# Optimization experiments

Measured on AMD Instinct MI355X. Metric: run time of the kernel, lower is better.

## Reference

```python
import jax, jax.numpy as jnp
import numpy as np
import math

S, B, H, NH, HD = 2048, 1, 4096, 32, 128
ROT = HD // 2  # 2D RoPE: each half of head_dim gets its own rotary embedding


def _rotate_half(x):
    x1, x2 = jnp.split(x, 2, axis=-1)
    return jnp.concatenate((-x2, x1), axis=-1)


def _rope_tables(max_pos, dim):
    inv_freq = 1.0 / (10000.0 ** (jnp.arange(0, dim, 2, dtype=jnp.float32) / dim))
    freqs = jnp.arange(max_pos, dtype=jnp.float32)[:, None] * inv_freq[None, :]  # [P, dim/2]
    emb = jnp.concatenate((freqs, freqs), axis=-1)  # [P, dim]
    return jnp.cos(emb), jnp.sin(emb)


def _apply_rope(q, k, cos_t, sin_t, pid):
    # q,k: [S,B,NH,ROT]; pid: [S,B]
    c = cos_t[pid][:, :, None, :]  # [S,B,1,ROT]
    s = sin_t[pid][:, :, None, :]
    return q * c + _rotate_half(q) * s, k * c + _rotate_half(k) * s


def setup_inputs() -> dict:
    key = jax.random.key(0)
    k1, k2, k3, k4, k5 = jax.random.split(key, 5)
    hidden_states = jax.random.normal(k1, (S, B, H), dtype=jnp.float32)
    pos = jnp.arange(S, dtype=jnp.int32)[None, :]          # [1,S] standard positions
    blk = jnp.zeros((1, S), dtype=jnp.int32)                # block positions (pre-gmask all zeros)
    position_ids = jnp.stack([pos, blk], axis=1)            # [B,2,S]
    # causal mask: True = masked out
    attention_mask = jnp.triu(jnp.ones((S, S), dtype=bool), k=1)[None, None]  # [B,1,S,S]
    Wqkv = jax.random.normal(k2, (3 * H, H), dtype=jnp.float32) * 0.02
    bqkv = jax.random.normal(k3, (3 * H,), dtype=jnp.float32) * 0.02
    Wd = jax.random.normal(k4, (H, H), dtype=jnp.float32) * 0.02
    bd = jax.random.normal(k5, (H,), dtype=jnp.float32) * 0.02
    return {"hidden_states": hidden_states, "position_ids": position_ids,
            "attention_mask": attention_mask, "layer_id": 5,
            "Wqkv": Wqkv, "bqkv": bqkv, "Wd": Wd, "bd": bd}


def reference(hidden_states, position_ids, attention_mask, layer_id, Wqkv, bqkv, Wd, bd):
    # QKV projection: [S,B,H] -> [S,B,NH,3*HD]
    mixed = hidden_states @ Wqkv.T + bqkv
    mixed = mixed.reshape(S, B, NH, 3 * HD)
    q, k, v = jnp.split(mixed, 3, axis=-1)  # each [S,B,NH,HD]

    # 2D rotary position embedding on the two head-dim halves
    q1, q2 = jnp.split(q, 2, axis=-1)
    k1, k2 = jnp.split(k, 2, axis=-1)
    cos_t, sin_t = _rope_tables(S, ROT)
    pid = position_ids[:, 0, :].T   # [S,B]
    bid = position_ids[:, 1, :].T   # [S,B]
    q1, k1 = _apply_rope(q1, k1, cos_t, sin_t, pid)
    q2, k2 = _apply_rope(q2, k2, cos_t, sin_t, bid)
    q = jnp.concatenate([q1, q2], axis=-1)
    k = jnp.concatenate([k1, k2], axis=-1)

    # layer-scaled attention scores
    coeff = float(layer_id + 1)
    q = q / (math.sqrt(HD) * coeff)
    scores = jnp.einsum('sbnd,tbnd->bnst', q, k)  # [B,NH,S,S]
    scores = jnp.where(attention_mask, jnp.float32(-10000.0), scores)
    scores = scores.astype(jnp.float32) * coeff
    probs = jax.nn.softmax(scores, axis=-1).astype(hidden_states.dtype)

    ctx = jnp.einsum('bnst,tbnd->sbnd', probs, v).reshape(S, B, NH * HD)
    return ctx @ Wd.T + bd  # [S,B,H]
```

## Files before the change

kernel.cpp:

```cpp
#include <hip/hip_runtime.h>


#define S_LEN 2048
#define NHEAD 32
#define HDIM 128
#define HID 4096

typedef float f32x4 __attribute__((ext_vector_type(4)));
typedef __bf16 bf16x8 __attribute__((ext_vector_type(8)));
typedef __bf16 bf16x4 __attribute__((ext_vector_type(4)));
typedef _Float16 f16x4 __attribute__((ext_vector_type(4)));
typedef _Float16 f16x8 __attribute__((ext_vector_type(8)));

__device__ __forceinline__ void gload16(const void* g, void* l) {
  __builtin_amdgcn_global_load_lds(
      (const __attribute__((address_space(1))) void*)g,
      (__attribute__((address_space(3))) void*)l, 16, 0, 0);
}

__global__ __launch_bounds__(256) void cvt_f32_bf16_kernel(
    const float* __restrict__ in, __bf16* __restrict__ out, int n4) {
  int i = blockIdx.x * 256 + threadIdx.x;
  if (i >= n4) return;
  f32x4 v = *(const f32x4*)(in + (size_t)i * 4);
  bf16x4 o;
  o[0] = (__bf16)v[0]; o[1] = (__bf16)v[1];
  o[2] = (__bf16)v[2]; o[3] = (__bf16)v[3];
  *(bf16x4*)(out + (size_t)i * 4) = o;
}

template <int UNITS>
__device__ __forceinline__ void stage_rows(const __bf16* __restrict__ G,
                                           int grow0, int Kstride, int kofs,
                                           __bf16* lds, int tid) {
#pragma unroll
  for (int i = 0; i < UNITS; ++i) {
    int idx = i * 512 + tid;
    int rr = idx >> 3;
    int offp = (idx & 7) * 16;
    int off = offp ^ ((rr & 7) << 4);
    const char* src =
        (const char*)(G + (size_t)(grow0 + rr) * Kstride + kofs) + off;
    char* dst = (char*)lds + idx * 16;
    gload16(src, dst);
  }
}

__device__ __forceinline__ bf16x8 ldsfrag(const __bf16* hb, int rowin, int ks,
                                          int lg) {
  int off = ((ks * 64 + lg * 16) ^ ((rowin & 7) << 4));
  return *(const bf16x8*)((const char*)hb + rowin * 128 + off);
}

#define BAR asm volatile("s_barrier" ::: "memory");

__global__ __launch_bounds__(512, 2) void gemm192_kernel(
    const __bf16* __restrict__ A, const __bf16* __restrict__ B,
    const float* __restrict__ bias, __bf16* __restrict__ Cout, int M, int N,
    int K, int mtiles) {
  __shared__ __align__(16) __bf16 As[2][256 * 64];
  __shared__ __align__(16) __bf16 Bs[2][192 * 64];
  const int tid = threadIdx.x;
  int bid = blockIdx.x;
  int per_patch = mtiles * 8;
  int p = bid / per_patch, r = bid % per_patch;
  int mt = r % mtiles, nt = p * 8 + r / mtiles;
  int m0 = mt * 256, n0 = nt * 192;
  const int wid = tid >> 6, l = tid & 63;
  const int wm = wid >> 1, wn = wid & 1;
  const int lr = l & 15, lg = l >> 4;
  const int nk = K >> 6;

  f32x4 acc[4][6];
#pragma unroll
  for (int a = 0; a < 4; ++a)
#pragma unroll
    for (int b = 0; b < 6; ++b) acc[a][b] = 0.f;

  stage_rows<4>(A, m0, K, 0, &As[0][0], tid);
  stage_rows<3>(B, n0, K, 0, &Bs[0][0], tid);
  stage_rows<4>(A, m0, K, 64, &As[1][0], tid);
  stage_rows<3>(B, n0, K, 64, &Bs[1][0], tid);
  asm volatile("s_waitcnt vmcnt(7)" ::: "memory");
  BAR;

  for (int t = 0; t < nk; ++t) {
    const int cur = t & 1;
    const int kt2 = (t + 2) * 64;
    const bool s2 = (t + 2 < nk);
    bf16x8 a0[4], b0[6], a1[4], b1[6];

#pragma unroll
    for (int mi = 0; mi < 4; ++mi)
      a0[mi] = ldsfrag(&As[cur][0], wm * 64 + mi * 16 + lr, 0, lg);
#pragma unroll
    for (int nj = 0; nj < 6; ++nj)
      b0[nj] = ldsfrag(&Bs[cur][0], wn * 96 + nj * 16 + lr, 0, lg);
    BAR;
    __builtin_amdgcn_s_setprio(1);
#pragma unroll
    for (int mi = 0; mi < 4; ++mi)
#pragma unroll
      for (int nj = 0; nj < 6; ++nj)
        acc[mi][nj] = __builtin_amdgcn_mfma_f32_16x16x32_bf16(
            a0[mi], b0[nj], acc[mi][nj], 0, 0, 0);
    __builtin_amdgcn_s_setprio(0);

#pragma unroll
    for (int mi = 0; mi < 4; ++mi)
      a1[mi] = ldsfrag(&As[cur][0], wm * 64 + mi * 16 + lr, 1, lg);
#pragma unroll
    for (int nj = 0; nj < 6; ++nj)
      b1[nj] = ldsfrag(&Bs[cur][0], wn * 96 + nj * 16 + lr, 1, lg);
    BAR;
    if (s2) {
      stage_rows<4>(A, m0, K, kt2, &As[cur][0], tid);
      stage_rows<3>(B, n0, K, kt2, &Bs[cur][0], tid);
    }
    __builtin_amdgcn_s_setprio(1);
#pragma unroll
    for (int mi = 0; mi < 4; ++mi)
#pragma unroll
      for (int nj = 0; nj < 6; ++nj)
        acc[mi][nj] = __builtin_amdgcn_mfma_f32_16x16x32_bf16(
            a1[mi], b1[nj], acc[mi][nj], 0, 0, 0);
    __builtin_amdgcn_s_setprio(0);
    if (s2)
      asm volatile("s_waitcnt vmcnt(7)" ::: "memory");
    else
      asm volatile("s_waitcnt vmcnt(0)" ::: "memory");
  }

#pragma unroll
  for (int mi = 0; mi < 4; ++mi)
#pragma unroll
    for (int nj = 0; nj < 6; ++nj) {
      int row = m0 + wm * 64 + mi * 16 + lg * 4;
      int col = n0 + wn * 96 + nj * 16 + lr;
      float bv = bias[col];
      f32x4 v = acc[mi][nj];
#pragma unroll
      for (int j = 0; j < 4; ++j)
        Cout[(size_t)(row + j) * N + col] = (__bf16)(v[j] + bv);
    }
}

__global__ __launch_bounds__(512, 2) void gemm128_kernel(
    const __bf16* __restrict__ A, const __bf16* __restrict__ B,
    const float* __restrict__ bias, float* __restrict__ Cout, int M, int N,
    int K, int mtiles) {
  __shared__ __align__(16) __bf16 As[2][128 * 64];
  __shared__ __align__(16) __bf16 Bs[2][2][128 * 64];
  const int tid = threadIdx.x;
  int bid = blockIdx.x;
  int per_patch = mtiles * 8;
  int p = bid / per_patch, r = bid % per_patch;
  int mt = r % mtiles, nt = p * 8 + r / mtiles;
  int m0 = mt * 128, n0 = nt * 256;
  const int wid = tid >> 6, l = tid & 63;
  const int wm = wid >> 2, wn = wid & 3;
  const int lr = l & 15, lg = l >> 4;
  const int nk = K >> 6;

  f32x4 acc[4][4];
#pragma unroll
  for (int a = 0; a < 4; ++a)
#pragma unroll
    for (int b = 0; b < 4; ++b) acc[a][b] = 0.f;

  const int bhalf = wn >> 1;
  const int br0 = (wn & 1) * 64;

  stage_rows<2>(A, m0, K, 0, &As[0][0], tid);
  stage_rows<2>(B, n0, K, 0, &Bs[0][0][0], tid);
  stage_rows<2>(B, n0 + 128, K, 0, &Bs[0][1][0], tid);
  stage_rows<2>(A, m0, K, 64, &As[1][0], tid);
  stage_rows<2>(B, n0, K, 64, &Bs[1][0][0], tid);
  stage_rows<2>(B, n0 + 128, K, 64, &Bs[1][1][0], tid);
  asm volatile("s_waitcnt vmcnt(6)" ::: "memory");
  BAR;

  for (int t = 0; t < nk; ++t) {
    const int cur = t & 1;
    const int kt2 = (t + 2) * 64;
    const bool s2 = (t + 2 < nk);
    const __bf16* bslot = &Bs[cur][bhalf][0];
    bf16x8 a0[4], b0[4], a1[4], b1[4];

#pragma unroll
    for (int mi = 0; mi < 4; ++mi)
      a0[mi] = ldsfrag(&As[cur][0], wm * 64 + mi * 16 + lr, 0, lg);
#pragma unroll
    for (int nj = 0; nj < 4; ++nj)
      b0[nj] = ldsfrag(bslot, br0 + nj * 16 + lr, 0, lg);
    BAR;
    __builtin_amdgcn_s_setprio(1);
#pragma unroll
    for (int mi = 0; mi < 4; ++mi)
#pragma unroll
      for (int nj = 0; nj < 4; ++nj)
        acc[mi][nj] = __builtin_amdgcn_mfma_f32_16x16x32_bf16(
            a0[mi], b0[nj], acc[mi][nj], 0, 0, 0);
    __builtin_amdgcn_s_setprio(0);

#pragma unroll
    for (int mi = 0; mi < 4; ++mi)
      a1[mi] = ldsfrag(&As[cur][0], wm * 64 + mi * 16 + lr, 1, lg);
#pragma unroll
    for (int nj = 0; nj < 4; ++nj)
      b1[nj] = ldsfrag(bslot, br0 + nj * 16 + lr, 1, lg);
    BAR;
    if (s2) {
      stage_rows<2>(A, m0, K, kt2, &As[cur][0], tid);
      stage_rows<2>(B, n0, K, kt2, &Bs[cur][0][0], tid);
      stage_rows<2>(B, n0 + 128, K, kt2, &Bs[cur][1][0], tid);
    }
    __builtin_amdgcn_s_setprio(1);
#pragma unroll
    for (int mi = 0; mi < 4; ++mi)
#pragma unroll
      for (int nj = 0; nj < 4; ++nj)
        acc[mi][nj] = __builtin_amdgcn_mfma_f32_16x16x32_bf16(
            a1[mi], b1[nj], acc[mi][nj], 0, 0, 0);
    __builtin_amdgcn_s_setprio(0);
    if (s2)
      asm volatile("s_waitcnt vmcnt(6)" ::: "memory");
    else
      asm volatile("s_waitcnt vmcnt(0)" ::: "memory");
  }

#pragma unroll
  for (int mi = 0; mi < 4; ++mi)
#pragma unroll
    for (int nj = 0; nj < 4; ++nj) {
      int row = m0 + wm * 64 + mi * 16 + lg * 4;
      int col = n0 + wn * 64 + nj * 16 + lr;
      float bv = bias[col];
      f32x4 v = acc[mi][nj];
#pragma unroll
      for (int j = 0; j < 4; ++j)
        Cout[(size_t)(row + j) * N + col] = v[j] + bv;
    }
}

__global__ __launch_bounds__(256) void rope_kernel(
    const __bf16* __restrict__ qkv, const int* __restrict__ pos_ids,
    __bf16* __restrict__ Q, __bf16* __restrict__ K, _Float16* __restrict__ VT) {
  int h = blockIdx.x & 31, sb = blockIdx.x >> 5;
  int s0 = sb * 64;
  int t = threadIdx.x;
  __shared__ float cs[64][2][2][32];
  __shared__ _Float16 vs[64][132];

  for (int idx = t; idx < 64 * 64; idx += 256) {
    int sl = idx >> 6, half = (idx >> 5) & 1, i = idx & 31;
    int p = pos_ids[half * S_LEN + s0 + sl];
    float f = powf(10000.f, -(float)i / 32.f);
    float ang = (float)p * f;
    cs[sl][half][0][i] = cosf(ang);
    cs[sl][half][1][i] = sinf(ang);
  }
#pragma unroll
  for (int c = 0; c < 4; c++) {
    int chunk = c * 256 + t;
    int slv = chunk >> 4, co = (chunk & 15) * 8;
    const __bf16* vsrc =
        qkv + (size_t)(s0 + slv) * (NHEAD * 3 * HDIM) + h * 384 + 256 + co;
    bf16x8 vv = *(const bf16x8*)vsrc;
    f16x4 a, b;
#pragma unroll
    for (int j = 0; j < 4; j++) {
      a[j] = (_Float16)(float)vv[j];
      b[j] = (_Float16)(float)vv[4 + j];
    }
    *(f16x4*)&vs[slv][co] = a;
    *(f16x4*)&vs[slv][co + 4] = b;
  }
  __syncthreads();

  {
    int sl = t >> 2, role = t & 3;
    int isK = role >> 1, half = role & 1;
    const __bf16* src = qkv + (size_t)(s0 + sl) * (NHEAD * 3 * HDIM) + h * 384 +
                        isK * 128 + half * 64;
    float scale = isK ? 1.f : 0.08838834764831845f;
    float x[64];
    bf16x8 buf[8];
#pragma unroll
    for (int c = 0; c < 8; c++) buf[c] = *(const bf16x8*)(src + c * 8);
#pragma unroll
    for (int c = 0; c < 8; c++)
#pragma unroll
      for (int j = 0; j < 8; j++) x[c * 8 + j] = (float)buf[c][j];
    bf16x8 ob[8];
#pragma unroll
    for (int i = 0; i < 64; i++) {
      int ii = i & 31;
      float cv = cs[sl][half][0][ii], sv = cs[sl][half][1][ii];
      float partner = (i < 32) ? x[i + 32] : x[i - 32];
      float sgn = (i < 32) ? -1.f : 1.f;
      float o = (x[i] * cv + sgn * partner * sv) * scale;
      ob[i >> 3][i & 7] = (__bf16)o;
    }
    __bf16* dst = (isK ? K : Q) + ((size_t)h * S_LEN + s0 + sl) * HDIM + half * 64;
#pragma unroll
    for (int c = 0; c < 8; c++) *(bf16x8*)(dst + c * 8) = ob[c];
  }

#pragma unroll
  for (int c = 0; c < 4; c++) {
    int chunk = c * 256 + t;
    int d = chunk >> 3, so = (chunk & 7) * 8;
    f16x8 o;
#pragma unroll
    for (int j = 0; j < 8; j++) o[j] = vs[so + j][d];
    *(f16x8*)(VT + ((size_t)h * HDIM + d) * S_LEN + s0 + so) = o;
  }
}

__global__ __launch_bounds__(256, 2) void attn_kernel(
    const __bf16* __restrict__ Q, const __bf16* __restrict__ K,
    const _Float16* __restrict__ VT, __bf16* __restrict__ ctx) {
  int b = blockIdx.x;
  int h = b & 31;
  int x = b >> 5;
  int qb = (b < 256) ? (15 - x) : (x - 8);
  int w = threadIdx.x >> 6, l = threadIdx.x & 63;
  int lr = l & 15, lg = l >> 4;
  int q0 = qb * 128 + w * 32;
  const __bf16* Qh = Q + (size_t)h * S_LEN * HDIM;
  const __bf16* Kh = K + (size_t)h * S_LEN * HDIM;
  const _Float16* Vh = VT + (size_t)h * HDIM * S_LEN;

  bf16x8 qfA[4], qfB[4];
#pragma unroll
  for (int kk = 0; kk < 4; kk++) {
    qfA[kk] = *(const bf16x8*)(Qh + (size_t)(q0 + lr) * HDIM + kk * 32 + lg * 8);
    qfB[kk] =
        *(const bf16x8*)(Qh + (size_t)(q0 + 16 + lr) * HDIM + kk * 32 + lg * 8);
  }

  f32x4 accA[8], accB[8];
#pragma unroll
  for (int tt = 0; tt < 8; tt++) { accA[tt] = 0.f; accB[tt] = 0.f; }
  float mA = -INFINITY, lsA = 0.f, mB = -INFINITY, lsB = 0.f;
  int qgA = q0 + lr, qgB = q0 + 16 + lr;
  int qmax = q0 + 31;

  for (int kv0 = 0; kv0 <= qmax; kv0 += 32) {
    f32x4 stA0 = 0.f, stA1 = 0.f, stB0 = 0.f, stB1 = 0.f;
#pragma unroll
    for (int kk = 0; kk < 4; kk++) {
      bf16x8 kf0 =
          *(const bf16x8*)(Kh + (size_t)(kv0 + lr) * HDIM + kk * 32 + lg * 8);
      bf16x8 kf1 = *(const bf16x8*)(Kh + (size_t)(kv0 + 16 + lr) * HDIM +
                                    kk * 32 + lg * 8);
      stA0 = __builtin_amdgcn_mfma_f32_16x16x32_bf16(kf0, qfA[kk], stA0, 0, 0, 0);
      stB0 = __builtin_amdgcn_mfma_f32_16x16x32_bf16(kf0, qfB[kk], stB0, 0, 0, 0);
      stA1 = __builtin_amdgcn_mfma_f32_16x16x32_bf16(kf1, qfA[kk], stA1, 0, 0, 0);
      stB1 = __builtin_amdgcn_mfma_f32_16x16x32_bf16(kf1, qfB[kk], stB1, 0, 0, 0);
    }

    f16x4 vb0[8], vb1[8];
#pragma unroll
    for (int tt = 0; tt < 8; tt++) {
      const _Float16* vcol = Vh + (size_t)(tt * 16 + lr) * S_LEN;
      vb0[tt] = *(const f16x4*)(vcol + kv0 + lg * 4);
      vb1[tt] = *(const f16x4*)(vcol + kv0 + 16 + lg * 4);
    }

    float tmA = -INFINITY, tmB = -INFINITY;
#pragma unroll
    for (int j = 0; j < 4; j++) {
      int kvg0 = kv0 + lg * 4 + j;
      int kvg1 = kvg0 + 16;
      if (kvg0 > qgA) stA0[j] = -INFINITY;
      if (kvg1 > qgA) stA1[j] = -INFINITY;
      if (kvg0 > qgB) stB0[j] = -INFINITY;
      if (kvg1 > qgB) stB1[j] = -INFINITY;
      tmA = fmaxf(tmA, fmaxf(stA0[j], stA1[j]));
      tmB = fmaxf(tmB, fmaxf(stB0[j], stB1[j]));
    }
    tmA = fmaxf(tmA, __shfl_xor(tmA, 16));
    tmA = fmaxf(tmA, __shfl_xor(tmA, 32));
    tmB = fmaxf(tmB, __shfl_xor(tmB, 16));
    tmB = fmaxf(tmB, __shfl_xor(tmB, 32));
    int need = __any((tmA > mA) || (tmB > mB));
    float mnA = fmaxf(mA, tmA), mnB = fmaxf(mB, tmB);

    f16x4 paA0, paA1, paB0, paB1;
    float tsA = 0.f, tsB = 0.f;
#pragma unroll
    for (int j = 0; j < 4; j++) {
      float pA0 = __expf(stA0[j] - mnA);
      float pA1 = __expf(stA1[j] - mnA);
      float pB0 = __expf(stB0[j] - mnB);
      float pB1 = __expf(stB1[j] - mnB);
      tsA += pA0 + pA1;
      tsB += pB0 + pB1;
      paA0[j] = (_Float16)pA0; paA1[j] = (_Float16)pA1;
      paB0[j] = (_Float16)pB0; paB1[j] = (_Float16)pB1;
    }
    tsA += __shfl_xor(tsA, 16);
    tsA += __shfl_xor(tsA, 32);
    tsB += __shfl_xor(tsB, 16);
    tsB += __shfl_xor(tsB, 32);

    if (need) {
      float scA = __expf(mA - mnA), scB = __expf(mB - mnB);
      lsA = lsA * scA + tsA;
      lsB = lsB * scB + tsB;
      float sAj[4], sBj[4];
#pragma unroll
      for (int j = 0; j < 4; j++) {
        sAj[j] = __shfl(scA, lg * 4 + j);
        sBj[j] = __shfl(scB, lg * 4 + j);
      }
#pragma unroll
      for (int tt = 0; tt < 8; tt++)
#pragma unroll
        for (int j = 0; j < 4; j++) {
          accA[tt][j] *= sAj[j];
          accB[tt][j] *= sBj[j];
        }
    } else {
      lsA += tsA;
      lsB += tsB;
    }
    mA = mnA; mB = mnB;

#pragma unroll
    for (int tt = 0; tt < 8; tt++) {
      accA[tt] =
          __builtin_amdgcn_mfma_f32_16x16x16f16(paA0, vb0[tt], accA[tt], 0, 0, 0);
      accB[tt] =
          __builtin_amdgcn_mfma_f32_16x16x16f16(paB0, vb0[tt], accB[tt], 0, 0, 0);
      accA[tt] =
          __builtin_amdgcn_mfma_f32_16x16x16f16(paA1, vb1[tt], accA[tt], 0, 0, 0);
      accB[tt] =
          __builtin_amdgcn_mfma_f32_16x16x16f16(paB1, vb1[tt], accB[tt], 0, 0, 0);
    }
  }

  float rA[4], rB[4];
#pragma unroll
  for (int j = 0; j < 4; j++) {
    rA[j] = 1.f / __shfl(lsA, lg * 4 + j);
    rB[j] = 1.f / __shfl(lsB, lg * 4 + j);
  }
#pragma unroll
  for (int tt = 0; tt < 8; tt++) {
#pragma unroll
    for (int j = 0; j < 4; j++) {
      int qoA = q0 + lg * 4 + j;
      int qoB = q0 + 16 + lg * 4 + j;
      ctx[(size_t)qoA * (NHEAD * HDIM) + h * HDIM + tt * 16 + lr] =
          (__bf16)(accA[tt][j] * rA[j]);
      ctx[(size_t)qoB * (NHEAD * HDIM) + h * HDIM + tt * 16 + lr] =
          (__bf16)(accB[tt][j] * rB[j]);
    }
  }
}

extern "C" void kernel_launch(void* const* d_in, const int* in_sizes, int n_in,
                              void* d_out, int out_size, void* d_ws,
                              size_t ws_size, hipStream_t stream) {
  const float* hs = (const float*)d_in[0];
  const int* pos_ids = (const int*)d_in[1];
  const float* Wqkv = (const float*)d_in[4];
  const float* bqkv = (const float*)d_in[5];
  const float* Wd = (const float*)d_in[6];
  const float* bd = (const float*)d_in[7];
  float* out = (float*)d_out;

  char* ws = (char*)d_ws;
  constexpr size_t OFF_W = 16777216ULL;
  constexpr size_t OFF_QKV = OFF_W + 100663296ULL;
  constexpr size_t OFF_Q = OFF_QKV + 50331648ULL;
  constexpr size_t OFF_K = OFF_Q + 16777216ULL;
  constexpr size_t OFF_V = OFF_K + 16777216ULL;
  __bf16* hsb = (__bf16*)(ws);
  __bf16* wqkvb = (__bf16*)(ws + OFF_W);
  __bf16* wdb = (__bf16*)(ws + OFF_W);
  __bf16* qkvb = (__bf16*)(ws + OFF_QKV);
  __bf16* ctxb = qkvb;
  __bf16* Qb = (__bf16*)(ws + OFF_Q);
  __bf16* Kb = (__bf16*)(ws + OFF_K);
  _Float16* Vtb = (_Float16*)(ws + OFF_V);

  cvt_f32_bf16_kernel<<<(S_LEN * HID) / 4 / 256, 256, 0, stream>>>(
      hs, hsb, S_LEN * HID / 4);
  cvt_f32_bf16_kernel<<<(3 * HID * HID) / 4 / 256, 256, 0, stream>>>(
      Wqkv, wqkvb, 3 * HID * HID / 4);

  gemm192_kernel<<<8 * 64, 512, 0, stream>>>(hsb, wqkvb, bqkv, qkvb, S_LEN,
                                             3 * HID, HID, 8);

  cvt_f32_bf16_kernel<<<(HID * HID) / 4 / 256, 256, 0, stream>>>(
      Wd, wdb, HID * HID / 4);

  rope_kernel<<<NHEAD * (S_LEN / 64), 256, 0, stream>>>(qkvb, pos_ids, Qb, Kb,
                                                        Vtb);

  attn_kernel<<<NHEAD * (S_LEN / 128), 256, 0, stream>>>(Qb, Kb, Vtb, ctxb);

  gemm128_kernel<<<16 * 16, 512, 0, stream>>>(ctxb, wdb, bd, out, S_LEN, HID,
                                              HID, 16);
}
```

Measured before the change: 580.7 us.

## Retile QKV GEMM to 256x256 quadrant pipeline and fold weight conversions

The QKV projection GEMM moves from 256x192 tiles to 256x256 tiles. Each K-step is split into four 128x128 quadrant MFMA phases, and the next stage's global-to-LDS loads are interleaved between those phases to improve operand reuse and overlap. The two fp32-to-bf16 conversions that feed the GEMM are merged into one launch. The Wd conversion now runs as 128 extra blocks of the attention kernel, which removes a separate launch and overlaps it with attention. Risks: the grid becomes 384 large blocks, which may leave a partial second wave, and the LDS footprint grows to 128KB per block.

Result: no change. 576.1 us (-0.8%).

```diff
diff --git a/kernel.cpp b/kernel.cpp
--- a/kernel.cpp
+++ b/kernel.cpp
@@ -18,15 +18,23 @@
       (__attribute__((address_space(3))) void*)l, 16, 0, 0);
 }
 
-__global__ __launch_bounds__(256) void cvt_f32_bf16_kernel(
-    const float* __restrict__ in, __bf16* __restrict__ out, int n4) {
-  int i = blockIdx.x * 256 + threadIdx.x;
-  if (i >= n4) return;
+__device__ __forceinline__ void cvt4(const float* in, __bf16* out, int i) {
   f32x4 v = *(const f32x4*)(in + (size_t)i * 4);
   bf16x4 o;
   o[0] = (__bf16)v[0]; o[1] = (__bf16)v[1];
   o[2] = (__bf16)v[2]; o[3] = (__bf16)v[3];
   *(bf16x4*)(out + (size_t)i * 4) = o;
+}
+
+__global__ __launch_bounds__(256) void cvt2_kernel(
+    const float* __restrict__ in1, __bf16* __restrict__ out1, int n4_1,
+    const float* __restrict__ in2, __bf16* __restrict__ out2, int n4_2) {
+  int i = blockIdx.x * 256 + threadIdx.x;
+  if (i < n4_1) {
+    cvt4(in1, out1, i);
+  } else if (i - n4_1 < n4_2) {
+    cvt4(in2, out2, i - n4_1);
+  }
 }
 
 template <int UNITS>
@@ -52,97 +60,117 @@
   return *(const bf16x8*)((const char*)hb + rowin * 128 + off);
 }
 
+#define READ_A(DST, SLOT)                                                     \
+  _Pragma("unroll") for (int mi = 0; mi < 4; ++mi)                            \
+      _Pragma("unroll") for (int ks = 0; ks < 2; ++ks) DST[mi][ks] =          \
+      ldsfrag(SLOT, wm * 64 + mi * 16 + lr, ks, lg);
+
+#define READ_B(DST, SLOT)                                                     \
+  _Pragma("unroll") for (int nj = 0; nj < 2; ++nj)                            \
+      _Pragma("unroll") for (int ks = 0; ks < 2; ++ks) DST[nj][ks] =          \
+      ldsfrag(SLOT, wn * 32 + nj * 16 + lr, ks, lg);
+
+#define MFMA_Q(MH, NH, AFR, BFR)                                              \
+  __builtin_amdgcn_s_setprio(1);                                              \
+  _Pragma("unroll") for (int mi = 0; mi < 4; ++mi)                            \
+      _Pragma("unroll") for (int nj = 0; nj < 2; ++nj)                        \
+          _Pragma("unroll") for (int ks = 0; ks < 2; ++ks)                    \
+              acc[MH][NH][mi][nj] =                                           \
+      __builtin_amdgcn_mfma_f32_16x16x32_bf16(AFR[mi][ks], BFR[nj][ks],       \
+                                              acc[MH][NH][mi][nj], 0, 0, 0);  \
+  __builtin_amdgcn_s_setprio(0);
+
 #define BAR asm volatile("s_barrier" ::: "memory");
 
-__global__ __launch_bounds__(512, 2) void gemm192_kernel(
+__global__ __launch_bounds__(512, 2) void gemm256_kernel(
     const __bf16* __restrict__ A, const __bf16* __restrict__ B,
     const float* __restrict__ bias, __bf16* __restrict__ Cout, int M, int N,
     int K, int mtiles) {
-  __shared__ __align__(16) __bf16 As[2][256 * 64];
-  __shared__ __align__(16) __bf16 Bs[2][192 * 64];
+  __shared__ __align__(16) __bf16 As[2][2][128 * 64];
+  __shared__ __align__(16) __bf16 Bs[2][2][128 * 64];
   const int tid = threadIdx.x;
   int bid = blockIdx.x;
   int per_patch = mtiles * 8;
   int p = bid / per_patch, r = bid % per_patch;
   int mt = r % mtiles, nt = p * 8 + r / mtiles;
-  int m0 = mt * 256, n0 = nt * 192;
+  int m0 = mt * 256, n0 = nt * 256;
   const int wid = tid >> 6, l = tid & 63;
-  const int wm = wid >> 1, wn = wid & 1;
+  const int wm = wid >> 2, wn = wid & 3;
   const int lr = l & 15, lg = l >> 4;
   const int nk = K >> 6;
 
-  f32x4 acc[4][6];
-#pragma unroll
-  for (int a = 0; a < 4; ++a)
-#pragma unroll
-    for (int b = 0; b < 6; ++b) acc[a][b] = 0.f;
-
-  stage_rows<4>(A, m0, K, 0, &As[0][0], tid);
-  stage_rows<3>(B, n0, K, 0, &Bs[0][0], tid);
-  stage_rows<4>(A, m0, K, 64, &As[1][0], tid);
-  stage_rows<3>(B, n0, K, 64, &Bs[1][0], tid);
-  asm volatile("s_waitcnt vmcnt(7)" ::: "memory");
+  f32x4 acc[2][2][4][2];
+#pragma unroll
+  for (int a = 0; a < 2; ++a)
+#pragma unroll
+    for (int b = 0; b < 2; ++b)
+#pragma unroll
+      for (int c = 0; c < 4; ++c)
+#pragma unroll
+        for (int d = 0; d < 2; ++d) acc[a][b][c][d] = 0.f;
+
+  stage_rows<2>(A, m0, K, 0, &As[0][0][0], tid);
+  stage_rows<2>(B, n0, K, 0, &Bs[0][0][0], tid);
+  stage_rows<2>(B, n0 + 128, K, 0, &Bs[0][1][0], tid);
+  stage_rows<2>(A, m0 + 128, K, 0, &As[0][1][0], tid);
+  if (nk > 1) {
+    stage_rows<2>(A, m0, K, 64, &As[1][0][0], tid);
+    stage_rows<2>(B, n0, K, 64, &Bs[1][0][0], tid);
+    stage_rows<2>(B, n0 + 128, K, 64, &Bs[1][1][0], tid);
+    asm volatile("s_waitcnt vmcnt(6)" ::: "memory");
+  } else {
+    asm volatile("s_waitcnt vmcnt(0)" ::: "memory");
+  }
   BAR;
 
   for (int t = 0; t < nk; ++t) {
-    const int cur = t & 1;
+    const int cur = t & 1, nxt = cur ^ 1;
+    const int kt1 = (t + 1) * 64;
     const int kt2 = (t + 2) * 64;
-    const bool s2 = (t + 2 < nk);
-    bf16x8 a0[4], b0[6], a1[4], b1[6];
-
-#pragma unroll
-    for (int mi = 0; mi < 4; ++mi)
-      a0[mi] = ldsfrag(&As[cur][0], wm * 64 + mi * 16 + lr, 0, lg);
-#pragma unroll
-    for (int nj = 0; nj < 6; ++nj)
-      b0[nj] = ldsfrag(&Bs[cur][0], wn * 96 + nj * 16 + lr, 0, lg);
+    const bool s1 = (t + 1 < nk), s2 = (t + 2 < nk);
+    bf16x8 a[4][2], b0[2][2], b1[2][2];
+
+    READ_A(a, &As[cur][0][0]);
+    READ_B(b0, &Bs[cur][0][0]);
+    if (s1) stage_rows<2>(A, m0 + 128, K, kt1, &As[nxt][1][0], tid);
     BAR;
-    __builtin_amdgcn_s_setprio(1);
-#pragma unroll
-    for (int mi = 0; mi < 4; ++mi)
-#pragma unroll
-      for (int nj = 0; nj < 6; ++nj)
-        acc[mi][nj] = __builtin_amdgcn_mfma_f32_16x16x32_bf16(
-            a0[mi], b0[nj], acc[mi][nj], 0, 0, 0);
-    __builtin_amdgcn_s_setprio(0);
-
-#pragma unroll
-    for (int mi = 0; mi < 4; ++mi)
-      a1[mi] = ldsfrag(&As[cur][0], wm * 64 + mi * 16 + lr, 1, lg);
-#pragma unroll
-    for (int nj = 0; nj < 6; ++nj)
-      b1[nj] = ldsfrag(&Bs[cur][0], wn * 96 + nj * 16 + lr, 1, lg);
+    MFMA_Q(0, 0, a, b0);
+
+    READ_B(b1, &Bs[cur][1][0]);
+    if (s2) stage_rows<2>(A, m0, K, kt2, &As[cur][0][0], tid);
     BAR;
-    if (s2) {
-      stage_rows<4>(A, m0, K, kt2, &As[cur][0], tid);
-      stage_rows<3>(B, n0, K, kt2, &Bs[cur][0], tid);
-    }
-    __builtin_amdgcn_s_setprio(1);
-#pragma unroll
-    for (int mi = 0; mi < 4; ++mi)
-#pragma unroll
-      for (int nj = 0; nj < 6; ++nj)
-        acc[mi][nj] = __builtin_amdgcn_mfma_f32_16x16x32_bf16(
-            a1[mi], b1[nj], acc[mi][nj], 0, 0, 0);
-    __builtin_amdgcn_s_setprio(0);
+    MFMA_Q(0, 1, a, b1);
+
+    READ_A(a, &As[cur][1][0]);
+    if (s2) stage_rows<2>(B, n0 + 128, K, kt2, &Bs[cur][1][0], tid);
+    BAR;
+    MFMA_Q(1, 1, a, b1);
+
+    if (s2) stage_rows<2>(B, n0, K, kt2, &Bs[cur][0][0], tid);
+    BAR;
+    MFMA_Q(1, 0, a, b0);
     if (s2)
-      asm volatile("s_waitcnt vmcnt(7)" ::: "memory");
+      asm volatile("s_waitcnt vmcnt(6)" ::: "memory");
     else
       asm volatile("s_waitcnt vmcnt(0)" ::: "memory");
   }
 
 #pragma unroll
-  for (int mi = 0; mi < 4; ++mi)
-#pragma unroll
-    for (int nj = 0; nj < 6; ++nj) {
-      int row = m0 + wm * 64 + mi * 16 + lg * 4;
-      int col = n0 + wn * 96 + nj * 16 + lr;
-      float bv = bias[col];
-      f32x4 v = acc[mi][nj];
-#pragma unroll
-      for (int j = 0; j < 4; ++j)
-        Cout[(size_t)(row + j) * N + col] = (__bf16)(v[j] + bv);
-    }
+  for (int mh = 0; mh < 2; ++mh)
+#pragma unroll
+    for (int nh = 0; nh < 2; ++nh)
+#pragma unroll
+      for (int mi = 0; mi < 4; ++mi)
+#pragma unroll
+        for (int nj = 0; nj < 2; ++nj) {
+          int row = m0 + mh * 128 + wm * 64 + mi * 16 + lg * 4;
+          int col = n0 + nh * 128 + wn * 32 + nj * 16 + lr;
+          float bv = bias[col];
+          f32x4 v = acc[mh][nh][mi][nj];
+#pragma unroll
+          for (int j = 0; j < 4; ++j)
+            Cout[(size_t)(row + j) * N + col] = (__bf16)(v[j] + bv);
+        }
 }
 
 __global__ __launch_bounds__(512, 2) void gemm128_kernel(
@@ -320,8 +348,15 @@
 
 __global__ __launch_bounds__(256, 2) void attn_kernel(
     const __bf16* __restrict__ Q, const __bf16* __restrict__ K,
-    const _Float16* __restrict__ VT, __bf16* __restrict__ ctx) {
+    const _Float16* __restrict__ VT, __bf16* __restrict__ ctx,
+    const float* __restrict__ Wd, __bf16* __restrict__ wdb) {
   int b = blockIdx.x;
+  if (b >= 512) {
+    const int n4 = HID * HID / 4;
+    for (int i = (b - 512) * 256 + threadIdx.x; i < n4; i += 128 * 256)
+      cvt4(Wd, wdb, i);
+    return;
+  }
   int h = b & 31;
   int x = b >> 5;
   int qb = (b < 256) ? (15 - x) : (x - 8);
@@ -488,21 +523,18 @@
   __bf16* Kb = (__bf16*)(ws + OFF_K);
   _Float16* Vtb = (_Float16*)(ws + OFF_V);
 
-  cvt_f32_bf16_kernel<<<(S_LEN * HID) / 4 / 256, 256, 0, stream>>>(
-      hs, hsb, S_LEN * HID / 4);
-  cvt_f32_bf16_kernel<<<(3 * HID * HID) / 4 / 256, 256, 0, stream>>>(
-      Wqkv, wqkvb, 3 * HID * HID / 4);
-
-  gemm192_kernel<<<8 * 64, 512, 0, stream>>>(hsb, wqkvb, bqkv, qkvb, S_LEN,
+  const int n4_hs = S_LEN * HID / 4;
+  const int n4_w = 3 * HID * HID / 4;
+  cvt2_kernel<<<(n4_hs + n4_w + 255) / 256, 256, 0, stream>>>(
+      hs, hsb, n4_hs, Wqkv, wqkvb, n4_w);
+
+  gemm256_kernel<<<8 * 48, 512, 0, stream>>>(hsb, wqkvb, bqkv, qkvb, S_LEN,
                                              3 * HID, HID, 8);
-
-  cvt_f32_bf16_kernel<<<(HID * HID) / 4 / 256, 256, 0, stream>>>(
-      Wd, wdb, HID * HID / 4);
 
   rope_kernel<<<NHEAD * (S_LEN / 64), 256, 0, stream>>>(qkvb, pos_ids, Qb, Kb,
                                                         Vtb);
 
-  attn_kernel<<<NHEAD * (S_LEN / 128), 256, 0, stream>>>(Qb, Kb, Vtb, ctxb);
+  attn_kernel<<<512 + 128, 256, 0, stream>>>(Qb, Kb, Vtb, ctxb, Wd, wdb);
 
   gemm128_kernel<<<16 * 16, 512, 0, stream>>>(ctxb, wdb, bd, out, S_LEN, HID,
                                               HID, 16);
```
